# Optimization experiments

Measured on AMD Instinct MI355X. Metric: run time of the kernel, lower is better.

## Reference

```python
import jax, jax.numpy as jnp
import numpy as np

NB_HEADS = 4
EMBED_DIM = 128
EPS = 1e-06


def setup_inputs() -> dict:
    key = jax.random.key(0)
    ks = jax.random.split(key, 9)
    B, R, C, E = 2, 64, 2048, 128
    s = 1.0 / np.sqrt(E)
    inp = {
        "input": jax.random.normal(ks[0], (B, R, C, E), dtype=jnp.float32),
        # weights stored as (in, out); torch Linear applies x @ W.T + b, equivalent here
        "Wq": jax.random.normal(ks[1], (E, E), dtype=jnp.float32) * s,
        "bq": jax.random.normal(ks[2], (E,), dtype=jnp.float32) * 0.01,
        "Wk": jax.random.normal(ks[3], (E, E), dtype=jnp.float32) * s,
        "bk": jax.random.normal(ks[4], (E,), dtype=jnp.float32) * 0.01,
        "Wv": jax.random.normal(ks[5], (E, E), dtype=jnp.float32) * s,
        "bv": jax.random.normal(ks[6], (E,), dtype=jnp.float32) * 0.01,
        "Wo": jax.random.normal(ks[7], (E, E), dtype=jnp.float32) * s,
        "bo": jax.random.normal(ks[8], (E,), dtype=jnp.float32) * 0.01,
    }
    return inp


def reference(input, Wq, bq, Wk, bk, Wv, bv, Wo, bo):
    B, R, C, E = input.shape
    H = NB_HEADS
    Dh = E // H
    # projections, split into heads: (B, R, C, H, Dh)
    q = (input @ Wq + bq).reshape(B, R, C, H, Dh)
    k = (input @ Wk + bk).reshape(B, R, C, H, Dh)
    v = (input @ Wv + bv).reshape(B, R, C, H, Dh)
    # elu+1 feature map
    q = jax.nn.elu(q) + 1.0
    k = jax.nn.elu(k) + 1.0
    # KtV: contract over col axis -> (B, R, H, Dh, Dh)
    KtV = jnp.einsum('brchd,brche->brhde', k, v)
    # normalizer: q . sum_c(k) -> (B, R, C, H)
    ksum = k.sum(axis=2)  # (B, R, H, Dh)
    Z = 1.0 / (jnp.einsum('brchd,brhd->brch', q, ksum) + EPS)
    # attention output: (B, R, C, H, Dh)
    out = jnp.einsum('brchd,brhde->brche', q, KtV) * Z[..., None]
    out = out.reshape(B, R, C, E)
    return out @ Wo + bo
```

## Files before the change

kernel.cpp:

```cpp
#include <hip/hip_runtime.h>

#define DEVINL __device__ __forceinline__

typedef __attribute__((ext_vector_type(8))) __bf16 bf16x8;
typedef __attribute__((ext_vector_type(4))) __bf16 bf16x4;
typedef __attribute__((ext_vector_type(4))) float f32x4;

DEVINL f32x4 mfma16(bf16x8 a, bf16x8 b, f32x4 c) {
  return __builtin_amdgcn_mfma_f32_16x16x32_bf16(a, b, c, 0, 0, 0);
}

DEVINL bf16x8 loadWfrag(const float* __restrict__ W, int kb, int n) {
  bf16x8 f;
#pragma unroll
  for (int j = 0; j < 8; ++j) f[j] = (__bf16)W[(kb + j) * 128 + n];
  return f;
}

__global__ __launch_bounds__(256, 2)
void qkv_ktv_kernel(const float* __restrict__ X,
                    const float* __restrict__ Wq, const float* __restrict__ bq,
                    const float* __restrict__ Wk, const float* __restrict__ bk,
                    const float* __restrict__ Wv, const float* __restrict__ bv,
                    __bf16* __restrict__ Qout,
                    float* __restrict__ ktvWs, float* __restrict__ ksumWs)
{
  __shared__ __bf16 Xs[64 * 136];
  __shared__ __bf16 Kt[128 * 72];
  __shared__ __bf16 Vt[128 * 72];

  const int tid  = threadIdx.x;
  const int lane = tid & 63;
  const int w    = tid >> 6;
  const int l15  = lane & 15;
  const int quad = lane >> 4;
  const int s     = blockIdx.x >> 2;
  const int chunk = blockIdx.x & 3;
  const int tokc0 = chunk * 512;
  const float* Xseq = X + (size_t)s * 2048 * 128;

  bf16x8 wkF[2][4], wvF[2][4], wqF[2][4];
#pragma unroll
  for (int nt = 0; nt < 2; ++nt) {
    const int n = w * 32 + nt * 16 + l15;
#pragma unroll
    for (int kk = 0; kk < 4; ++kk) {
      const int kb = kk * 32 + quad * 8;
      wkF[nt][kk] = loadWfrag(Wk, kb, n);
      wvF[nt][kk] = loadWfrag(Wv, kb, n);
      wqF[nt][kk] = loadWfrag(Wq, kb, n);
    }
  }
  float bkr[2], bvr[2], bqr[2][4];
#pragma unroll
  for (int nt = 0; nt < 2; ++nt) {
    bkr[nt] = bk[w * 32 + nt * 16 + l15];
    bvr[nt] = bv[w * 32 + nt * 16 + l15];
#pragma unroll
    for (int r = 0; r < 4; ++r)
      bqr[nt][r] = bq[w * 32 + nt * 16 + quad * 4 + r];
  }

  f32x4 accT[2][2] = {};
  float ksumAcc[2] = {0.f, 0.f};

  for (int t = 0; t < 8; ++t) {
    const float* Xtile = Xseq + (size_t)(tokc0 + t * 64) * 128;
    __syncthreads();
#pragma unroll
    for (int i = 0; i < 8; ++i) {
      const int flat = tid + i * 256;
      const int row = flat >> 5;
      const int c4  = (flat & 31) * 4;
      const float4 v = *(const float4*)(Xtile + row * 128 + c4);
      bf16x4 b4;
      b4[0] = (__bf16)v.x; b4[1] = (__bf16)v.y;
      b4[2] = (__bf16)v.z; b4[3] = (__bf16)v.w;
      *(bf16x4*)(&Xs[row * 136 + c4]) = b4;
    }
    __syncthreads();

#pragma unroll
    for (int mt = 0; mt < 4; ++mt) {
      f32x4 aK[2] = {}, aV[2] = {};
#pragma unroll
      for (int kk = 0; kk < 4; ++kk) {
        const bf16x8 ax = *(const bf16x8*)(&Xs[(mt * 16 + l15) * 136 + kk * 32 + quad * 8]);
        aK[0] = mfma16(ax, wkF[0][kk], aK[0]);
        aK[1] = mfma16(ax, wkF[1][kk], aK[1]);
        aV[0] = mfma16(ax, wvF[0][kk], aV[0]);
        aV[1] = mfma16(ax, wvF[1][kk], aV[1]);
      }
#pragma unroll
      for (int nt = 0; nt < 2; ++nt) {
        const int e    = w * 32 + nt * 16 + l15;
        const int tokb = mt * 16 + quad * 4;
        bf16x4 kq, vq;
        float ks = 0.f;
#pragma unroll
        for (int r = 0; r < 4; ++r) {
          float kv = aK[nt][r] + bkr[nt];
          kv = (kv > 0.f) ? (kv + 1.f) : __expf(kv);
          ks += kv;
          kq[r] = (__bf16)kv;
          vq[r] = (__bf16)(aV[nt][r] + bvr[nt]);
        }
        ksumAcc[nt] += ks;
        *(bf16x4*)(&Kt[e * 72 + tokb]) = kq;
        *(bf16x4*)(&Vt[e * 72 + tokb]) = vq;
      }
    }

#pragma unroll
    for (int ntq = 0; ntq < 4; ++ntq) {
      f32x4 aQ[2] = {};
#pragma unroll
      for (int kk = 0; kk < 4; ++kk) {
        const bf16x8 bx = *(const bf16x8*)(&Xs[(ntq * 16 + l15) * 136 + kk * 32 + quad * 8]);
        aQ[0] = mfma16(wqF[0][kk], bx, aQ[0]);
        aQ[1] = mfma16(wqF[1][kk], bx, aQ[1]);
      }
      const int tok = tokc0 + t * 64 + ntq * 16 + l15;
      __bf16* qrow = Qout + ((size_t)s * 2048 + tok) * 128;
#pragma unroll
      for (int mt = 0; mt < 2; ++mt) {
        bf16x4 qq;
#pragma unroll
        for (int r = 0; r < 4; ++r) {
          float qv = aQ[mt][r] + bqr[mt][r];
          qv = (qv > 0.f) ? (qv + 1.f) : __expf(qv);
          qq[r] = (__bf16)qv;
        }
        *(bf16x4*)(qrow + w * 32 + mt * 16 + quad * 4) = qq;
      }
    }
    __syncthreads();

#pragma unroll
    for (int kk = 0; kk < 2; ++kk) {
      bf16x8 aF[2], bF[2];
#pragma unroll
      for (int dt = 0; dt < 2; ++dt)
        aF[dt] = *(const bf16x8*)(&Kt[(w * 32 + dt * 16 + l15) * 72 + kk * 32 + quad * 8]);
#pragma unroll
      for (int et = 0; et < 2; ++et)
        bF[et] = *(const bf16x8*)(&Vt[(w * 32 + et * 16 + l15) * 72 + kk * 32 + quad * 8]);
#pragma unroll
      for (int dt = 0; dt < 2; ++dt)
#pragma unroll
        for (int et = 0; et < 2; ++et)
          accT[dt][et] = mfma16(aF[dt], bF[et], accT[dt][et]);
    }
  }

  float* ktvH = ktvWs + ((size_t)s * 4 + w) * 1024;
#pragma unroll
  for (int dt = 0; dt < 2; ++dt)
#pragma unroll
    for (int et = 0; et < 2; ++et)
#pragma unroll
      for (int r = 0; r < 4; ++r)
        atomicAdd(&ktvH[(dt * 16 + quad * 4 + r) * 32 + et * 16 + l15], accT[dt][et][r]);

#pragma unroll
  for (int nt = 0; nt < 2; ++nt) {
    float v2 = ksumAcc[nt];
    v2 += __shfl_down(v2, 32);
    v2 += __shfl_down(v2, 16);
    if (quad == 0)
      atomicAdd(&ksumWs[s * 128 + w * 32 + nt * 16 + l15], v2);
  }
}

__global__ __launch_bounds__(256, 2)
void attn_out_kernel(const __bf16* __restrict__ Qin,
                     const float* __restrict__ ktvWs, const float* __restrict__ ksumWs,
                     const float* __restrict__ Wo, const float* __restrict__ bo,
                     float* __restrict__ Out)
{
  __shared__ __bf16 Qs[64 * 136];
  __shared__ __bf16 A2s[64 * 136];
  __shared__ float ksums[128];
  __shared__ float Zs[64 * 4];

  const int tid  = threadIdx.x;
  const int lane = tid & 63;
  const int w    = tid >> 6;
  const int l15  = lane & 15;
  const int quad = lane >> 4;
  const int s     = blockIdx.x >> 2;
  const int chunk = blockIdx.x & 3;

  if (tid < 128) ksums[tid] = ksumWs[s * 128 + tid];

  const float* ktvH = ktvWs + ((size_t)s * 4 + w) * 1024;
  bf16x8 aKtv[2];
#pragma unroll
  for (int mt = 0; mt < 2; ++mt)
#pragma unroll
    for (int j = 0; j < 8; ++j)
      aKtv[mt][j] = (__bf16)ktvH[(quad * 8 + j) * 32 + mt * 16 + l15];

  bf16x8 woF[2][4];
  float bor[2];
#pragma unroll
  for (int nt = 0; nt < 2; ++nt) {
    const int n = w * 32 + nt * 16 + l15;
    bor[nt] = bo[n];
#pragma unroll
    for (int kk = 0; kk < 4; ++kk)
      woF[nt][kk] = loadWfrag(Wo, kk * 32 + quad * 8, n);
  }
  __syncthreads();

  for (int t = 0; t < 8; ++t) {
    const int tok0 = chunk * 512 + t * 64;
    const __bf16* Qtile = Qin + ((size_t)s * 2048 + tok0) * 128;
    __syncthreads();
#pragma unroll
    for (int i = 0; i < 4; ++i) {
      const int c = tid + i * 256;
      const int row = c >> 4, cc = (c & 15) * 8;
      *(bf16x8*)(&Qs[row * 136 + cc]) = *(const bf16x8*)(Qtile + row * 128 + cc);
    }
    __syncthreads();
    {
      const int tok = tid >> 2, h = tid & 3;
      float dot = 0.f;
      const __bf16* qrow = &Qs[tok * 136 + h * 32];
      const float* ksrow = &ksums[h * 32];
#pragma unroll
      for (int j = 0; j < 32; ++j) dot += (float)qrow[j] * ksrow[j];
      Zs[tok * 4 + h] = 1.f / (dot + 1e-6f);
    }
    __syncthreads();
#pragma unroll
    for (int ntq = 0; ntq < 4; ++ntq) {
      const bf16x8 bq8 = *(const bf16x8*)(&Qs[(ntq * 16 + l15) * 136 + w * 32 + quad * 8]);
      f32x4 acc[2] = {};
      acc[0] = mfma16(aKtv[0], bq8, acc[0]);
      acc[1] = mfma16(aKtv[1], bq8, acc[1]);
      const int tokRow = ntq * 16 + l15;
      const float z = Zs[tokRow * 4 + w];
#pragma unroll
      for (int mt = 0; mt < 2; ++mt) {
        bf16x4 a4;
#pragma unroll
        for (int r = 0; r < 4; ++r) a4[r] = (__bf16)(acc[mt][r] * z);
        *(bf16x4*)(&A2s[tokRow * 136 + w * 32 + mt * 16 + quad * 4]) = a4;
      }
    }
    __syncthreads();
#pragma unroll
    for (int mt = 0; mt < 4; ++mt) {
      f32x4 acc[2] = {};
#pragma unroll
      for (int kk = 0; kk < 4; ++kk) {
        const bf16x8 aa = *(const bf16x8*)(&A2s[(mt * 16 + l15) * 136 + kk * 32 + quad * 8]);
        acc[0] = mfma16(aa, woF[0][kk], acc[0]);
        acc[1] = mfma16(aa, woF[1][kk], acc[1]);
      }
      const int tokb = tok0 + mt * 16 + quad * 4;
      float* orow = Out + ((size_t)s * 2048 + tokb) * 128;
#pragma unroll
      for (int nt = 0; nt < 2; ++nt) {
        const int n = w * 32 + nt * 16 + l15;
#pragma unroll
        for (int r = 0; r < 4; ++r)
          orow[(size_t)r * 128 + n] = acc[nt][r] + bor[nt];
      }
    }
  }
}

extern "C" void kernel_launch(void* const* d_in, const int* in_sizes, int n_in,
                              void* d_out, int out_size, void* d_ws, size_t ws_size,
                              hipStream_t stream) {
  const float* X  = (const float*)d_in[0];
  const float* Wq = (const float*)d_in[1];
  const float* bq = (const float*)d_in[2];
  const float* Wk = (const float*)d_in[3];
  const float* bk = (const float*)d_in[4];
  const float* Wv = (const float*)d_in[5];
  const float* bv = (const float*)d_in[6];
  const float* Wo = (const float*)d_in[7];
  const float* bo = (const float*)d_in[8];
  float* Out = (float*)d_out;

  const size_t Q_BYTES    = (size_t)128 * 2048 * 128 * 2;
  const size_t KTV_BYTES  = (size_t)128 * 4 * 32 * 32 * 4;
  const size_t KSUM_BYTES = (size_t)128 * 128 * 4;
  __bf16* Qws   = (__bf16*)d_ws;
  float* ktvWs  = (float*)((char*)d_ws + Q_BYTES);
  float* ksumWs = (float*)((char*)d_ws + Q_BYTES + KTV_BYTES);

  hipMemsetAsync((char*)d_ws + Q_BYTES, 0, KTV_BYTES + KSUM_BYTES, stream);

  qkv_ktv_kernel<<<dim3(512), dim3(256), 0, stream>>>(
      X, Wq, bq, Wk, bk, Wv, bv, Qws, ktvWs, ksumWs);
  attn_out_kernel<<<dim3(512), dim3(256), 0, stream>>>(
      Qws, ktvWs, ksumWs, Wo, bo, Out);
}
```

Before: 312.2 us.

## Split sequences across more blocks, prefetch tiles in registers, compute normalizer via MFMA

Both kernels now launch 2048 blocks of 128 tokens each instead of 512 blocks of 512 tokens, so more blocks are resident across the CUs. Launch bounds are raised to 3 and 4 waves per SIMD. The next X or Q tile is prefetched into registers while the current tile is processed, which hides global load latency and drops one barrier per iteration. The attention kernel now computes the normalizer Z with an extra MFMA against a ksum fragment instead of a separate shared-memory dot-product pass, removing that pass and two barriers. In exchange, more blocks perform atomic adds into the KtV/ksum workspace, register pressure rises, and ksum is rounded to bf16.

```diff
diff --git a/kernel.cpp b/kernel.cpp
--- a/kernel.cpp
+++ b/kernel.cpp
@@ -17,7 +17,7 @@
   return f;
 }
 
-__global__ __launch_bounds__(256, 2)
+__global__ __launch_bounds__(256, 3)
 void qkv_ktv_kernel(const float* __restrict__ X,
                     const float* __restrict__ Wq, const float* __restrict__ bq,
                     const float* __restrict__ Wk, const float* __restrict__ bk,
@@ -34,9 +34,9 @@
   const int w    = tid >> 6;
   const int l15  = lane & 15;
   const int quad = lane >> 4;
-  const int s     = blockIdx.x >> 2;
-  const int chunk = blockIdx.x & 3;
-  const int tokc0 = chunk * 512;
+  const int s     = blockIdx.x >> 4;
+  const int chunk = blockIdx.x & 15;
+  const int tokc0 = chunk * 128;
   const float* Xseq = X + (size_t)s * 2048 * 128;
 
   bf16x8 wkF[2][4], wvF[2][4], wqF[2][4];
@@ -64,21 +64,35 @@
   f32x4 accT[2][2] = {};
   float ksumAcc[2] = {0.f, 0.f};
 
-  for (int t = 0; t < 8; ++t) {
-    const float* Xtile = Xseq + (size_t)(tokc0 + t * 64) * 128;
-    __syncthreads();
+  float4 pf[8];
+  {
+    const float* Xtile = Xseq + (size_t)(tokc0) * 128;
 #pragma unroll
     for (int i = 0; i < 8; ++i) {
       const int flat = tid + i * 256;
-      const int row = flat >> 5;
-      const int c4  = (flat & 31) * 4;
-      const float4 v = *(const float4*)(Xtile + row * 128 + c4);
+      pf[i] = *(const float4*)(Xtile + (flat >> 5) * 128 + (flat & 31) * 4);
+    }
+  }
+
+  for (int t = 0; t < 2; ++t) {
+    __syncthreads();
+#pragma unroll
+    for (int i = 0; i < 8; ++i) {
+      const int flat = tid + i * 256;
       bf16x4 b4;
-      b4[0] = (__bf16)v.x; b4[1] = (__bf16)v.y;
-      b4[2] = (__bf16)v.z; b4[3] = (__bf16)v.w;
-      *(bf16x4*)(&Xs[row * 136 + c4]) = b4;
-    }
-    __syncthreads();
+      b4[0] = (__bf16)pf[i].x; b4[1] = (__bf16)pf[i].y;
+      b4[2] = (__bf16)pf[i].z; b4[3] = (__bf16)pf[i].w;
+      *(bf16x4*)(&Xs[(flat >> 5) * 136 + (flat & 31) * 4]) = b4;
+    }
+    __syncthreads();
+    if (t == 0) {
+      const float* Xtile = Xseq + (size_t)(tokc0 + 64) * 128;
+#pragma unroll
+      for (int i = 0; i < 8; ++i) {
+        const int flat = tid + i * 256;
+        pf[i] = *(const float4*)(Xtile + (flat >> 5) * 128 + (flat & 31) * 4);
+      }
+    }
 
 #pragma unroll
     for (int mt = 0; mt < 4; ++mt) {
@@ -134,7 +148,6 @@
         *(bf16x4*)(qrow + w * 32 + mt * 16 + quad * 4) = qq;
       }
     }
-    __syncthreads();
 
 #pragma unroll
     for (int kk = 0; kk < 2; ++kk) {
@@ -172,7 +185,7 @@
   }
 }
 
-__global__ __launch_bounds__(256, 2)
+__global__ __launch_bounds__(256, 4)
 void attn_out_kernel(const __bf16* __restrict__ Qin,
                      const float* __restrict__ ktvWs, const float* __restrict__ ksumWs,
                      const float* __restrict__ Wo, const float* __restrict__ bo,
@@ -180,18 +193,14 @@
 {
   __shared__ __bf16 Qs[64 * 136];
   __shared__ __bf16 A2s[64 * 136];
-  __shared__ float ksums[128];
-  __shared__ float Zs[64 * 4];
 
   const int tid  = threadIdx.x;
   const int lane = tid & 63;
   const int w    = tid >> 6;
   const int l15  = lane & 15;
   const int quad = lane >> 4;
-  const int s     = blockIdx.x >> 2;
-  const int chunk = blockIdx.x & 3;
-
-  if (tid < 128) ksums[tid] = ksumWs[s * 128 + tid];
+  const int s     = blockIdx.x >> 4;
+  const int chunk = blockIdx.x & 15;
 
   const float* ktvH = ktvWs + ((size_t)s * 4 + w) * 1024;
   bf16x8 aKtv[2];
@@ -200,6 +209,11 @@
 #pragma unroll
     for (int j = 0; j < 8; ++j)
       aKtv[mt][j] = (__bf16)ktvH[(quad * 8 + j) * 32 + mt * 16 + l15];
+
+  bf16x8 aKs;
+#pragma unroll
+  for (int j = 0; j < 8; ++j)
+    aKs[j] = (__bf16)ksumWs[s * 128 + w * 32 + quad * 8 + j];
 
   bf16x8 woF[2][4];
   float bor[2];
@@ -211,46 +225,55 @@
     for (int kk = 0; kk < 4; ++kk)
       woF[nt][kk] = loadWfrag(Wo, kk * 32 + quad * 8, n);
   }
-  __syncthreads();
-
-  for (int t = 0; t < 8; ++t) {
-    const int tok0 = chunk * 512 + t * 64;
-    const __bf16* Qtile = Qin + ((size_t)s * 2048 + tok0) * 128;
-    __syncthreads();
+
+  const __bf16* Qseq = Qin + (size_t)s * 2048 * 128;
+  bf16x8 qpf[4];
+  {
+    const __bf16* Qtile = Qseq + (size_t)(chunk * 128) * 128;
 #pragma unroll
     for (int i = 0; i < 4; ++i) {
       const int c = tid + i * 256;
-      const int row = c >> 4, cc = (c & 15) * 8;
-      *(bf16x8*)(&Qs[row * 136 + cc]) = *(const bf16x8*)(Qtile + row * 128 + cc);
-    }
-    __syncthreads();
-    {
-      const int tok = tid >> 2, h = tid & 3;
-      float dot = 0.f;
-      const __bf16* qrow = &Qs[tok * 136 + h * 32];
-      const float* ksrow = &ksums[h * 32];
-#pragma unroll
-      for (int j = 0; j < 32; ++j) dot += (float)qrow[j] * ksrow[j];
-      Zs[tok * 4 + h] = 1.f / (dot + 1e-6f);
-    }
-    __syncthreads();
+      qpf[i] = *(const bf16x8*)(Qtile + (c >> 4) * 128 + (c & 15) * 8);
+    }
+  }
+
+  for (int t = 0; t < 2; ++t) {
+    const int tok0 = chunk * 128 + t * 64;
+    __syncthreads();
+#pragma unroll
+    for (int i = 0; i < 4; ++i) {
+      const int c = tid + i * 256;
+      *(bf16x8*)(&Qs[(c >> 4) * 136 + (c & 15) * 8]) = qpf[i];
+    }
+    __syncthreads();
+    if (t == 0) {
+      const __bf16* Qtile = Qseq + (size_t)(chunk * 128 + 64) * 128;
+#pragma unroll
+      for (int i = 0; i < 4; ++i) {
+        const int c = tid + i * 256;
+        qpf[i] = *(const bf16x8*)(Qtile + (c >> 4) * 128 + (c & 15) * 8);
+      }
+    }
+
 #pragma unroll
     for (int ntq = 0; ntq < 4; ++ntq) {
       const bf16x8 bq8 = *(const bf16x8*)(&Qs[(ntq * 16 + l15) * 136 + w * 32 + quad * 8]);
-      f32x4 acc[2] = {};
-      acc[0] = mfma16(aKtv[0], bq8, acc[0]);
-      acc[1] = mfma16(aKtv[1], bq8, acc[1]);
+      f32x4 zero = {};
+      f32x4 accD = mfma16(aKs, bq8, zero);
+      f32x4 acc0 = mfma16(aKtv[0], bq8, zero);
+      f32x4 acc1 = mfma16(aKtv[1], bq8, zero);
+      const float z = 1.f / (accD[0] + 1e-6f);
       const int tokRow = ntq * 16 + l15;
-      const float z = Zs[tokRow * 4 + w];
-#pragma unroll
-      for (int mt = 0; mt < 2; ++mt) {
-        bf16x4 a4;
-#pragma unroll
-        for (int r = 0; r < 4; ++r) a4[r] = (__bf16)(acc[mt][r] * z);
-        *(bf16x4*)(&A2s[tokRow * 136 + w * 32 + mt * 16 + quad * 4]) = a4;
-      }
-    }
-    __syncthreads();
+      bf16x4 a4;
+#pragma unroll
+      for (int r = 0; r < 4; ++r) a4[r] = (__bf16)(acc0[r] * z);
+      *(bf16x4*)(&A2s[tokRow * 136 + w * 32 + quad * 4]) = a4;
+#pragma unroll
+      for (int r = 0; r < 4; ++r) a4[r] = (__bf16)(acc1[r] * z);
+      *(bf16x4*)(&A2s[tokRow * 136 + w * 32 + 16 + quad * 4]) = a4;
+    }
+    __syncthreads();
+
 #pragma unroll
     for (int mt = 0; mt < 4; ++mt) {
       f32x4 acc[2] = {};
@@ -296,8 +319,8 @@
 
   hipMemsetAsync((char*)d_ws + Q_BYTES, 0, KTV_BYTES + KSUM_BYTES, stream);
 
-  qkv_ktv_kernel<<<dim3(512), dim3(256), 0, stream>>>(
+  qkv_ktv_kernel<<<dim3(2048), dim3(256), 0, stream>>>(
       X, Wq, bq, Wk, bk, Wv, bv, Qws, ktvWs, ksumWs);
-  attn_out_kernel<<<dim3(512), dim3(256), 0, stream>>>(
+  attn_out_kernel<<<dim3(2048), dim3(256), 0, stream>>>(
       Qws, ktvWs, ksumWs, Wo, bo, Out);
 }
```

After: 482.0 us. +54.4%, slower.

## Recompute Q in output kernel instead of round-tripping it through global memory

Applied to the files above, without the earlier changes.

Splits work so the first kernel only computes K/V projections and KtV/ksum, while the second kernel recomputes the Q projection from X and fuses it with the attention and output projection. This removes the bf16 Q workspace write and read, at the cost of reading X a second time. The normalizer is now computed with an MFMA against ksum instead of a scalar dot loop, and the grid is doubled to 1024 blocks with half the tokens each, which doubles the atomic reductions.

```diff
diff --git a/kernel.cpp b/kernel.cpp
--- a/kernel.cpp
+++ b/kernel.cpp
@@ -18,12 +18,10 @@
 }
 
 __global__ __launch_bounds__(256, 2)
-void qkv_ktv_kernel(const float* __restrict__ X,
-                    const float* __restrict__ Wq, const float* __restrict__ bq,
-                    const float* __restrict__ Wk, const float* __restrict__ bk,
-                    const float* __restrict__ Wv, const float* __restrict__ bv,
-                    __bf16* __restrict__ Qout,
-                    float* __restrict__ ktvWs, float* __restrict__ ksumWs)
+void kv_ktv_kernel(const float* __restrict__ X,
+                   const float* __restrict__ Wk, const float* __restrict__ bk,
+                   const float* __restrict__ Wv, const float* __restrict__ bv,
+                   float* __restrict__ ktvWs, float* __restrict__ ksumWs)
 {
   __shared__ __bf16 Xs[64 * 136];
   __shared__ __bf16 Kt[128 * 72];
@@ -34,49 +32,42 @@
   const int w    = tid >> 6;
   const int l15  = lane & 15;
   const int quad = lane >> 4;
-  const int s     = blockIdx.x >> 2;
-  const int chunk = blockIdx.x & 3;
-  const int tokc0 = chunk * 512;
+  const int s     = blockIdx.x >> 3;
+  const int chunk = blockIdx.x & 7;
+  const int tokc0 = chunk * 256;
   const float* Xseq = X + (size_t)s * 2048 * 128;
 
-  bf16x8 wkF[2][4], wvF[2][4], wqF[2][4];
+  bf16x8 wkF[2][4], wvF[2][4];
 #pragma unroll
   for (int nt = 0; nt < 2; ++nt) {
     const int n = w * 32 + nt * 16 + l15;
 #pragma unroll
     for (int kk = 0; kk < 4; ++kk) {
-      const int kb = kk * 32 + quad * 8;
-      wkF[nt][kk] = loadWfrag(Wk, kb, n);
-      wvF[nt][kk] = loadWfrag(Wv, kb, n);
-      wqF[nt][kk] = loadWfrag(Wq, kb, n);
-    }
-  }
-  float bkr[2], bvr[2], bqr[2][4];
+      wkF[nt][kk] = loadWfrag(Wk, kk * 32 + quad * 8, n);
+      wvF[nt][kk] = loadWfrag(Wv, kk * 32 + quad * 8, n);
+    }
+  }
+  float bkr[2], bvr[2];
 #pragma unroll
   for (int nt = 0; nt < 2; ++nt) {
     bkr[nt] = bk[w * 32 + nt * 16 + l15];
     bvr[nt] = bv[w * 32 + nt * 16 + l15];
-#pragma unroll
-    for (int r = 0; r < 4; ++r)
-      bqr[nt][r] = bq[w * 32 + nt * 16 + quad * 4 + r];
   }
 
   f32x4 accT[2][2] = {};
   float ksumAcc[2] = {0.f, 0.f};
 
-  for (int t = 0; t < 8; ++t) {
+  for (int t = 0; t < 4; ++t) {
     const float* Xtile = Xseq + (size_t)(tokc0 + t * 64) * 128;
     __syncthreads();
 #pragma unroll
     for (int i = 0; i < 8; ++i) {
       const int flat = tid + i * 256;
-      const int row = flat >> 5;
-      const int c4  = (flat & 31) * 4;
-      const float4 v = *(const float4*)(Xtile + row * 128 + c4);
+      const float4 v = *(const float4*)(Xtile + (flat >> 5) * 128 + (flat & 31) * 4);
       bf16x4 b4;
       b4[0] = (__bf16)v.x; b4[1] = (__bf16)v.y;
       b4[2] = (__bf16)v.z; b4[3] = (__bf16)v.w;
-      *(bf16x4*)(&Xs[row * 136 + c4]) = b4;
+      *(bf16x4*)(&Xs[(flat >> 5) * 136 + (flat & 31) * 4]) = b4;
     }
     __syncthreads();
 
@@ -112,16 +103,113 @@
     }
 
 #pragma unroll
+    for (int kk = 0; kk < 2; ++kk) {
+      bf16x8 aF[2], bF[2];
+#pragma unroll
+      for (int dt = 0; dt < 2; ++dt)
+        aF[dt] = *(const bf16x8*)(&Kt[(w * 32 + dt * 16 + l15) * 72 + kk * 32 + quad * 8]);
+#pragma unroll
+      for (int et = 0; et < 2; ++et)
+        bF[et] = *(const bf16x8*)(&Vt[(w * 32 + et * 16 + l15) * 72 + kk * 32 + quad * 8]);
+#pragma unroll
+      for (int dt = 0; dt < 2; ++dt)
+#pragma unroll
+        for (int et = 0; et < 2; ++et)
+          accT[dt][et] = mfma16(aF[dt], bF[et], accT[dt][et]);
+    }
+  }
+
+  float* ktvH = ktvWs + ((size_t)s * 4 + w) * 1024;
+#pragma unroll
+  for (int dt = 0; dt < 2; ++dt)
+#pragma unroll
+    for (int et = 0; et < 2; ++et)
+#pragma unroll
+      for (int r = 0; r < 4; ++r)
+        atomicAdd(&ktvH[(dt * 16 + quad * 4 + r) * 32 + et * 16 + l15], accT[dt][et][r]);
+
+#pragma unroll
+  for (int nt = 0; nt < 2; ++nt) {
+    float v2 = ksumAcc[nt];
+    v2 += __shfl_down(v2, 32);
+    v2 += __shfl_down(v2, 16);
+    if (quad == 0)
+      atomicAdd(&ksumWs[s * 128 + w * 32 + nt * 16 + l15], v2);
+  }
+}
+
+__global__ __launch_bounds__(256, 2)
+void q_attn_out_kernel(const float* __restrict__ X,
+                       const float* __restrict__ Wq, const float* __restrict__ bq,
+                       const float* __restrict__ ktvWs, const float* __restrict__ ksumWs,
+                       const float* __restrict__ Wo, const float* __restrict__ bo,
+                       float* __restrict__ Out)
+{
+  __shared__ __bf16 XA[64 * 136];
+  __shared__ __bf16 Qs[64 * 136];
+
+  const int tid  = threadIdx.x;
+  const int lane = tid & 63;
+  const int w    = tid >> 6;
+  const int l15  = lane & 15;
+  const int quad = lane >> 4;
+  const int s     = blockIdx.x >> 3;
+  const int chunk = blockIdx.x & 7;
+  const float* Xseq = X + (size_t)s * 2048 * 128;
+
+  const float* ktvH = ktvWs + ((size_t)s * 4 + w) * 1024;
+  bf16x8 aKtv[2];
+#pragma unroll
+  for (int mt = 0; mt < 2; ++mt)
+#pragma unroll
+    for (int j = 0; j < 8; ++j)
+      aKtv[mt][j] = (__bf16)ktvH[(quad * 8 + j) * 32 + mt * 16 + l15];
+
+  bf16x8 aKs;
+#pragma unroll
+  for (int j = 0; j < 8; ++j)
+    aKs[j] = (__bf16)ksumWs[s * 128 + w * 32 + quad * 8 + j];
+
+  bf16x8 wqF[2][4], woF[2][4];
+  float bqr[2][4], bor[2];
+#pragma unroll
+  for (int nt = 0; nt < 2; ++nt) {
+    const int n = w * 32 + nt * 16 + l15;
+    bor[nt] = bo[n];
+#pragma unroll
+    for (int kk = 0; kk < 4; ++kk) {
+      wqF[nt][kk] = loadWfrag(Wq, kk * 32 + quad * 8, n);
+      woF[nt][kk] = loadWfrag(Wo, kk * 32 + quad * 8, n);
+    }
+#pragma unroll
+    for (int r = 0; r < 4; ++r)
+      bqr[nt][r] = bq[w * 32 + nt * 16 + quad * 4 + r];
+  }
+
+  for (int t = 0; t < 4; ++t) {
+    const int tok0 = chunk * 256 + t * 64;
+    __syncthreads();
+#pragma unroll
+    for (int i = 0; i < 8; ++i) {
+      const int flat = tid + i * 256;
+      const float4 v = *(const float4*)(Xseq + (size_t)tok0 * 128 + (flat >> 5) * 128 + (flat & 31) * 4);
+      bf16x4 b4;
+      b4[0] = (__bf16)v.x; b4[1] = (__bf16)v.y;
+      b4[2] = (__bf16)v.z; b4[3] = (__bf16)v.w;
+      *(bf16x4*)(&XA[(flat >> 5) * 136 + (flat & 31) * 4]) = b4;
+    }
+    __syncthreads();
+
+#pragma unroll
     for (int ntq = 0; ntq < 4; ++ntq) {
       f32x4 aQ[2] = {};
 #pragma unroll
       for (int kk = 0; kk < 4; ++kk) {
-        const bf16x8 bx = *(const bf16x8*)(&Xs[(ntq * 16 + l15) * 136 + kk * 32 + quad * 8]);
+        const bf16x8 bx = *(const bf16x8*)(&XA[(ntq * 16 + l15) * 136 + kk * 32 + quad * 8]);
         aQ[0] = mfma16(wqF[0][kk], bx, aQ[0]);
         aQ[1] = mfma16(wqF[1][kk], bx, aQ[1]);
       }
-      const int tok = tokc0 + t * 64 + ntq * 16 + l15;
-      __bf16* qrow = Qout + ((size_t)s * 2048 + tok) * 128;
+      const int tok = ntq * 16 + l15;
 #pragma unroll
       for (int mt = 0; mt < 2; ++mt) {
         bf16x4 qq;
@@ -131,132 +219,36 @@
           qv = (qv > 0.f) ? (qv + 1.f) : __expf(qv);
           qq[r] = (__bf16)qv;
         }
-        *(bf16x4*)(qrow + w * 32 + mt * 16 + quad * 4) = qq;
-      }
-    }
-    __syncthreads();
-
-#pragma unroll
-    for (int kk = 0; kk < 2; ++kk) {
-      bf16x8 aF[2], bF[2];
-#pragma unroll
-      for (int dt = 0; dt < 2; ++dt)
-        aF[dt] = *(const bf16x8*)(&Kt[(w * 32 + dt * 16 + l15) * 72 + kk * 32 + quad * 8]);
-#pragma unroll
-      for (int et = 0; et < 2; ++et)
-        bF[et] = *(const bf16x8*)(&Vt[(w * 32 + et * 16 + l15) * 72 + kk * 32 + quad * 8]);
-#pragma unroll
-      for (int dt = 0; dt < 2; ++dt)
-#pragma unroll
-        for (int et = 0; et < 2; ++et)
-          accT[dt][et] = mfma16(aF[dt], bF[et], accT[dt][et]);
-    }
-  }
-
-  float* ktvH = ktvWs + ((size_t)s * 4 + w) * 1024;
-#pragma unroll
-  for (int dt = 0; dt < 2; ++dt)
-#pragma unroll
-    for (int et = 0; et < 2; ++et)
-#pragma unroll
-      for (int r = 0; r < 4; ++r)
-        atomicAdd(&ktvH[(dt * 16 + quad * 4 + r) * 32 + et * 16 + l15], accT[dt][et][r]);
-
-#pragma unroll
-  for (int nt = 0; nt < 2; ++nt) {
-    float v2 = ksumAcc[nt];
-    v2 += __shfl_down(v2, 32);
-    v2 += __shfl_down(v2, 16);
-    if (quad == 0)
-      atomicAdd(&ksumWs[s * 128 + w * 32 + nt * 16 + l15], v2);
-  }
-}
-
-__global__ __launch_bounds__(256, 2)
-void attn_out_kernel(const __bf16* __restrict__ Qin,
-                     const float* __restrict__ ktvWs, const float* __restrict__ ksumWs,
-                     const float* __restrict__ Wo, const float* __restrict__ bo,
-                     float* __restrict__ Out)
-{
-  __shared__ __bf16 Qs[64 * 136];
-  __shared__ __bf16 A2s[64 * 136];
-  __shared__ float ksums[128];
-  __shared__ float Zs[64 * 4];
-
-  const int tid  = threadIdx.x;
-  const int lane = tid & 63;
-  const int w    = tid >> 6;
-  const int l15  = lane & 15;
-  const int quad = lane >> 4;
-  const int s     = blockIdx.x >> 2;
-  const int chunk = blockIdx.x & 3;
-
-  if (tid < 128) ksums[tid] = ksumWs[s * 128 + tid];
-
-  const float* ktvH = ktvWs + ((size_t)s * 4 + w) * 1024;
-  bf16x8 aKtv[2];
-#pragma unroll
-  for (int mt = 0; mt < 2; ++mt)
-#pragma unroll
-    for (int j = 0; j < 8; ++j)
-      aKtv[mt][j] = (__bf16)ktvH[(quad * 8 + j) * 32 + mt * 16 + l15];
-
-  bf16x8 woF[2][4];
-  float bor[2];
-#pragma unroll
-  for (int nt = 0; nt < 2; ++nt) {
-    const int n = w * 32 + nt * 16 + l15;
-    bor[nt] = bo[n];
-#pragma unroll
-    for (int kk = 0; kk < 4; ++kk)
-      woF[nt][kk] = loadWfrag(Wo, kk * 32 + quad * 8, n);
-  }
-  __syncthreads();
-
-  for (int t = 0; t < 8; ++t) {
-    const int tok0 = chunk * 512 + t * 64;
-    const __bf16* Qtile = Qin + ((size_t)s * 2048 + tok0) * 128;
-    __syncthreads();
-#pragma unroll
-    for (int i = 0; i < 4; ++i) {
-      const int c = tid + i * 256;
-      const int row = c >> 4, cc = (c & 15) * 8;
-      *(bf16x8*)(&Qs[row * 136 + cc]) = *(const bf16x8*)(Qtile + row * 128 + cc);
-    }
-    __syncthreads();
-    {
-      const int tok = tid >> 2, h = tid & 3;
-      float dot = 0.f;
-      const __bf16* qrow = &Qs[tok * 136 + h * 32];
-      const float* ksrow = &ksums[h * 32];
-#pragma unroll
-      for (int j = 0; j < 32; ++j) dot += (float)qrow[j] * ksrow[j];
-      Zs[tok * 4 + h] = 1.f / (dot + 1e-6f);
-    }
-    __syncthreads();
+        *(bf16x4*)(&Qs[tok * 136 + w * 32 + mt * 16 + quad * 4]) = qq;
+      }
+    }
+    __syncthreads();
+
 #pragma unroll
     for (int ntq = 0; ntq < 4; ++ntq) {
       const bf16x8 bq8 = *(const bf16x8*)(&Qs[(ntq * 16 + l15) * 136 + w * 32 + quad * 8]);
-      f32x4 acc[2] = {};
-      acc[0] = mfma16(aKtv[0], bq8, acc[0]);
-      acc[1] = mfma16(aKtv[1], bq8, acc[1]);
+      f32x4 zero = {};
+      f32x4 accD = mfma16(aKs, bq8, zero);
+      f32x4 acc0 = mfma16(aKtv[0], bq8, zero);
+      f32x4 acc1 = mfma16(aKtv[1], bq8, zero);
+      const float z = 1.f / (accD[0] + 1e-6f);
       const int tokRow = ntq * 16 + l15;
-      const float z = Zs[tokRow * 4 + w];
-#pragma unroll
-      for (int mt = 0; mt < 2; ++mt) {
-        bf16x4 a4;
-#pragma unroll
-        for (int r = 0; r < 4; ++r) a4[r] = (__bf16)(acc[mt][r] * z);
-        *(bf16x4*)(&A2s[tokRow * 136 + w * 32 + mt * 16 + quad * 4]) = a4;
-      }
-    }
-    __syncthreads();
+      bf16x4 a4;
+#pragma unroll
+      for (int r = 0; r < 4; ++r) a4[r] = (__bf16)(acc0[r] * z);
+      *(bf16x4*)(&XA[tokRow * 136 + w * 32 + quad * 4]) = a4;
+#pragma unroll
+      for (int r = 0; r < 4; ++r) a4[r] = (__bf16)(acc1[r] * z);
+      *(bf16x4*)(&XA[tokRow * 136 + w * 32 + 16 + quad * 4]) = a4;
+    }
+    __syncthreads();
+
 #pragma unroll
     for (int mt = 0; mt < 4; ++mt) {
       f32x4 acc[2] = {};
 #pragma unroll
       for (int kk = 0; kk < 4; ++kk) {
-        const bf16x8 aa = *(const bf16x8*)(&A2s[(mt * 16 + l15) * 136 + kk * 32 + quad * 8]);
+        const bf16x8 aa = *(const bf16x8*)(&XA[(mt * 16 + l15) * 136 + kk * 32 + quad * 8]);
         acc[0] = mfma16(aa, woF[0][kk], acc[0]);
         acc[1] = mfma16(aa, woF[1][kk], acc[1]);
       }
@@ -287,17 +279,15 @@
   const float* bo = (const float*)d_in[8];
   float* Out = (float*)d_out;
 
-  const size_t Q_BYTES    = (size_t)128 * 2048 * 128 * 2;
   const size_t KTV_BYTES  = (size_t)128 * 4 * 32 * 32 * 4;
   const size_t KSUM_BYTES = (size_t)128 * 128 * 4;
-  __bf16* Qws   = (__bf16*)d_ws;
-  float* ktvWs  = (float*)((char*)d_ws + Q_BYTES);
-  float* ksumWs = (float*)((char*)d_ws + Q_BYTES + KTV_BYTES);
-
-  hipMemsetAsync((char*)d_ws + Q_BYTES, 0, KTV_BYTES + KSUM_BYTES, stream);
-
-  qkv_ktv_kernel<<<dim3(512), dim3(256), 0, stream>>>(
-      X, Wq, bq, Wk, bk, Wv, bv, Qws, ktvWs, ksumWs);
-  attn_out_kernel<<<dim3(512), dim3(256), 0, stream>>>(
-      Qws, ktvWs, ksumWs, Wo, bo, Out);
-}
+  float* ktvWs  = (float*)d_ws;
+  float* ksumWs = (float*)((char*)d_ws + KTV_BYTES);
+
+  hipMemsetAsync(d_ws, 0, KTV_BYTES + KSUM_BYTES, stream);
+
+  kv_ktv_kernel<<<dim3(1024), dim3(256), 0, stream>>>(
+      X, Wk, bk, Wv, bv, ktvWs, ksumWs);
+  q_attn_out_kernel<<<dim3(1024), dim3(256), 0, stream>>>(
+      X, Wq, bq, ktvWs, ksumWs, Wo, bo, Out);
+}
```

Result: no change. 317.1 us (+1.6%).
